# Kernel tuning notes

Measured on AMD Instinct MI355X. Metric: run time of the kernel, lower is better.

The kernel has to match this reference:

```python
import jax, jax.numpy as jnp
import numpy as np

WIN = 5            # attn.window_size
K = 2 * WIN + 1    # max local window width
NEG = -10000.0


def gru_cell(x, h, w_ih, w_hh, b_ih, b_hh):
    # torch GRU cell: r,z,n gate order
    gi = x @ w_ih.T + b_ih
    gh = h @ w_hh.T + b_hh
    ir, iz, inn = jnp.split(gi, 3, axis=-1)
    hr, hz, hn = jnp.split(gh, 3, axis=-1)
    r = jax.nn.sigmoid(ir + hr)
    z = jax.nn.sigmoid(iz + hz)
    n = jnp.tanh(inn + r * hn)
    return (1.0 - z) * n + z * h


def setup_inputs() -> dict:
    key = jax.random.key(0)
    ks = jax.random.split(key, 26)
    B, S, V, E, H, Hd = 64, 1024, 50257, 300, 1000, 500
    sc = 0.05
    dec_in = jax.random.randint(ks[0], (B, 1), 0, V)
    lengths = jax.random.randint(ks[1], (B,), 64, S + 1)
    mask0 = jnp.arange(S)[None, :] < lengths[:, None]          # [B,S] bool pad mask
    enc_out = jax.random.normal(ks[2], (B, S, H), jnp.float32)
    attn_hidden = jax.random.normal(ks[3], (B, 1, H), jnp.float32) * sc
    h0 = jax.random.normal(ks[4], (4, B, Hd), jnp.float32) * sc  # [layers*dirs,B,Hd]
    embed = jax.random.normal(ks[5], (V, E), jnp.float32) * sc
    embed = embed.at[0].set(0.0)  # padding_idx=0
    # GRU layer0 (input = E+H due to input feeding), layer1 (input = H)
    w_ih0 = jax.random.normal(ks[6], (2, 3 * Hd, E + H), jnp.float32) * sc
    w_hh0 = jax.random.normal(ks[7], (2, 3 * Hd, Hd), jnp.float32) * sc
    b_ih0 = jax.random.normal(ks[8], (2, 3 * Hd), jnp.float32) * sc
    b_hh0 = jax.random.normal(ks[9], (2, 3 * Hd), jnp.float32) * sc
    w_ih1 = jax.random.normal(ks[10], (2, 3 * Hd, H), jnp.float32) * sc
    w_hh1 = jax.random.normal(ks[11], (2, 3 * Hd, Hd), jnp.float32) * sc
    b_ih1 = jax.random.normal(ks[12], (2, 3 * Hd), jnp.float32) * sc
    b_hh1 = jax.random.normal(ks[13], (2, 3 * Hd), jnp.float32) * sc
    Wp_w = jax.random.normal(ks[14], (H, H), jnp.float32) * sc
    Wp_b = jax.random.normal(ks[15], (H,), jnp.float32) * sc
    Vp_w = jax.random.normal(ks[16], (H, 1), jnp.float32) * sc
    Vp_b = jax.random.normal(ks[17], (1,), jnp.float32) * sc
    Wc_w = jax.random.normal(ks[18], (2 * H, H), jnp.float32) * sc
    Wc_b = jax.random.normal(ks[19], (H,), jnp.float32) * sc
    out_w = jax.random.normal(ks[20], (H, V), jnp.float32) * sc
    out_b = jax.random.normal(ks[21], (V,), jnp.float32) * sc
    return {
        'dec_in': dec_in, 'attn_hidden': attn_hidden, 'enc_out': enc_out,
        'mask0': mask0, 'lengths': lengths, 'h0': h0, 'embed': embed,
        'w_ih0': w_ih0, 'w_hh0': w_hh0, 'b_ih0': b_ih0, 'b_hh0': b_hh0,
        'w_ih1': w_ih1, 'w_hh1': w_hh1, 'b_ih1': b_ih1, 'b_hh1': b_hh1,
        'Wp_w': Wp_w, 'Wp_b': Wp_b, 'Vp_w': Vp_w, 'Vp_b': Vp_b,
        'Wc_w': Wc_w, 'Wc_b': Wc_b, 'out_w': out_w, 'out_b': out_b, 't': 0,
    }


def reference(dec_in, attn_hidden, enc_out, mask0, lengths, h0, embed,
              w_ih0, w_hh0, b_ih0, b_hh0, w_ih1, w_hh1, b_ih1, b_hh1,
              Wp_w, Wp_b, Vp_w, Vp_b, Wc_w, Wc_b, out_w, out_b, t):
    Smax = enc_out.shape[1]
    # embed + input feeding (seq len of the decoder step is 1)
    x = jnp.concatenate([embed[dec_in[:, 0]], attn_hidden[:, 0]], axis=-1)  # [B,E+H]
    # 2-layer bidirectional GRU over a length-1 sequence (eval: no dropout)
    hf = gru_cell(x, h0[0], w_ih0[0], w_hh0[0], b_ih0[0], b_hh0[0])
    hb = gru_cell(x, h0[1], w_ih0[1], w_hh0[1], b_ih0[1], b_hh0[1])
    x1 = jnp.concatenate([hf, hb], axis=-1)                                  # [B,H]
    hf2 = gru_cell(x1, h0[2], w_ih1[0], w_hh1[0], b_ih1[0], b_hh1[0])
    hb2 = gru_cell(x1, h0[3], w_ih1[1], w_hh1[1], b_ih1[1], b_hh1[1])
    ht = jnp.concatenate([hf2, hb2], axis=-1)[:, None, :]                    # [B,1,H]
    # local-p predictive window: pt = int(S * sigmoid(Vp(tanh(Wp(ht)))))
    Sf = lengths.astype(ht.dtype)
    pt = (Sf * jax.nn.sigmoid(jnp.tanh(ht @ Wp_w + Wp_b) @ Vp_w + Vp_b).reshape(-1)).astype(jnp.int32)
    p0 = jnp.minimum(lengths - WIN, jnp.maximum(0, pt - WIN))                # [B]
    p1 = jnp.minimum(lengths, pt + 1 + WIN)
    idx = p0[:, None] + jnp.arange(K)                                        # [B,K]
    valid = idx < p1[:, None]
    idxc = jnp.clip(idx, 0, Smax - 1)
    hs_w = jnp.take_along_axis(enc_out, idxc[:, :, None], axis=1)            # [B,K,H] batched gather
    m_w = jnp.take_along_axis(mask0, idxc, axis=1) & valid                   # [B,K]
    # dot alignment + mask + softmax
    a = jnp.einsum('bod,bkd->bok', ht, hs_w)                                 # [B,1,K]
    a = jax.nn.softmax(jnp.where(m_w[:, None, :], a, NEG), axis=-1)
    c = jnp.einsum('bok,bkd->bod', a, hs_w)                                  # [B,1,H]
    h_attn = jnp.tanh(jnp.concatenate([c, ht], axis=-1) @ Wc_w + Wc_b)       # [B,1,H]
    y = (h_attn @ out_w + out_b)[:, 0]                                       # [B,V]
    return jax.nn.log_softmax(y, axis=-1)
```

## Files before the change

### kernel.cpp

```cpp
#include <hip/hip_runtime.h>
#include <hip/hip_bf16.h>
#include <math.h>

typedef __attribute__((ext_vector_type(8))) short bf16x8;
typedef __attribute__((ext_vector_type(4))) float f32x4;

__device__ __forceinline__ float sigmoidf_(float x){ return 1.f/(1.f + expf(-x)); }
__device__ __forceinline__ short f2bf(float x){
    union { __hip_bfloat16 h; short s; } u; u.h = __float2bfloat16(x); return u.s;
}
__device__ __forceinline__ float bf2f(short s){
    union { unsigned u; float f; } v; v.u = ((unsigned)(unsigned short)s) << 16; return v.f;
}

template<int TRANS, int BIAS>
__device__ __forceinline__ void mm_core(
    const short* __restrict__ Abf, const float* __restrict__ W,
    const float* __restrict__ bias, float* __restrict__ outP,
    int K, int Kp, int N, int ks0, int ks1, int nblk)
{
    const int lane = threadIdx.x & 63;
    const int wave = threadIdx.x >> 6;
    const int l16  = lane & 15;
    const int lg   = lane >> 4;
    const int n    = nblk*64 + wave*16 + l16;
    const int nc   = min(n, N-1);

    f32x4 acc[4];
#pragma unroll
    for (int mt = 0; mt < 4; mt++) acc[mt] = f32x4{0.f,0.f,0.f,0.f};

    for (int ks = ks0; ks < ks1; ks++) {
        const int kl = ks*32 + lg*8;
        const short* ap = Abf + (long)l16*Kp + kl;
        bf16x8 a0 = *(const bf16x8*)(ap);
        bf16x8 a1 = *(const bf16x8*)(ap + (long)16*Kp);
        bf16x8 a2 = *(const bf16x8*)(ap + (long)32*Kp);
        bf16x8 a3 = *(const bf16x8*)(ap + (long)48*Kp);
        float wv[8];
        if (TRANS) {
            const float* wr = W + (long)nc*K;
            if (kl + 8 <= K) {
                float4 f0 = *(const float4*)(wr + kl);
                float4 f1 = *(const float4*)(wr + kl + 4);
                wv[0]=f0.x; wv[1]=f0.y; wv[2]=f0.z; wv[3]=f0.w;
                wv[4]=f1.x; wv[5]=f1.y; wv[6]=f1.z; wv[7]=f1.w;
            } else {
#pragma unroll
                for (int j=0;j<8;j++) wv[j] = wr[min(kl+j, K-1)];
            }
        } else {
            const float* wk = W + (long)kl*(long)N + nc;
            if (kl + 8 <= K) {
#pragma unroll
                for (int j=0;j<8;j++) wv[j] = wk[(long)j*N];
            } else {
#pragma unroll
                for (int j=0;j<8;j++) wv[j] = (kl+j < K) ? wk[(long)j*N] : 0.f;
            }
        }
        bf16x8 b;
#pragma unroll
        for (int j=0;j<8;j++) b[j] = f2bf(wv[j]);

        acc[0] = __builtin_amdgcn_mfma_f32_16x16x32_bf16(a0, b, acc[0], 0, 0, 0);
        acc[1] = __builtin_amdgcn_mfma_f32_16x16x32_bf16(a1, b, acc[1], 0, 0, 0);
        acc[2] = __builtin_amdgcn_mfma_f32_16x16x32_bf16(a2, b, acc[2], 0, 0, 0);
        acc[3] = __builtin_amdgcn_mfma_f32_16x16x32_bf16(a3, b, acc[3], 0, 0, 0);
    }

    if (n < N) {
        const float bv = BIAS ? bias[n] : 0.f;
#pragma unroll
        for (int mt = 0; mt < 4; mt++) {
#pragma unroll
            for (int q = 0; q < 4; q++) {
                int row = mt*16 + lg*4 + q;
                outP[(long)row*N + n] = acc[mt][q] + bv;
            }
        }
    }
}

template<int TRANS>
__device__ __forceinline__ void mm_core4(
    const short* __restrict__ Ahi, const short* __restrict__ Alo,
    const float* __restrict__ W, float* __restrict__ outP,
    int K, int Kp, int N, int ks0, int ks1, int nblk)
{
    const int lane = threadIdx.x & 63;
    const int wave = threadIdx.x >> 6;
    const int l16  = lane & 15;
    const int lg   = lane >> 4;
    const int n    = nblk*64 + wave*16 + l16;
    const int nc   = min(n, N-1);

    f32x4 acc[4];
#pragma unroll
    for (int mt = 0; mt < 4; mt++) acc[mt] = f32x4{0.f,0.f,0.f,0.f};

    for (int ks = ks0; ks < ks1; ks++) {
        const int kl = ks*32 + lg*8;
        const long o0 = (long)l16*Kp + kl;
        bf16x8 ah0 = *(const bf16x8*)(Ahi + o0);
        bf16x8 ah1 = *(const bf16x8*)(Ahi + o0 + (long)16*Kp);
        bf16x8 ah2 = *(const bf16x8*)(Ahi + o0 + (long)32*Kp);
        bf16x8 ah3 = *(const bf16x8*)(Ahi + o0 + (long)48*Kp);
        bf16x8 al0 = *(const bf16x8*)(Alo + o0);
        bf16x8 al1 = *(const bf16x8*)(Alo + o0 + (long)16*Kp);
        bf16x8 al2 = *(const bf16x8*)(Alo + o0 + (long)32*Kp);
        bf16x8 al3 = *(const bf16x8*)(Alo + o0 + (long)48*Kp);
        float wv[8];
        if (TRANS) {
            const float* wr = W + (long)nc*K;
            if (kl + 8 <= K) {
                float4 f0 = *(const float4*)(wr + kl);
                float4 f1 = *(const float4*)(wr + kl + 4);
                wv[0]=f0.x; wv[1]=f0.y; wv[2]=f0.z; wv[3]=f0.w;
                wv[4]=f1.x; wv[5]=f1.y; wv[6]=f1.z; wv[7]=f1.w;
            } else {
#pragma unroll
                for (int j=0;j<8;j++) wv[j] = wr[min(kl+j, K-1)];
            }
        } else {
            const float* wk = W + (long)kl*(long)N + nc;
            if (kl + 8 <= K) {
#pragma unroll
                for (int j=0;j<8;j++) wv[j] = wk[(long)j*N];
            } else {
#pragma unroll
                for (int j=0;j<8;j++) wv[j] = (kl+j < K) ? wk[(long)j*N] : 0.f;
            }
        }
        bf16x8 bh, bl;
#pragma unroll
        for (int j=0;j<8;j++) {
            short h = f2bf(wv[j]);
            bh[j] = h;
            bl[j] = f2bf(wv[j] - bf2f(h));
        }
        acc[0] = __builtin_amdgcn_mfma_f32_16x16x32_bf16(ah0, bh, acc[0], 0, 0, 0);
        acc[1] = __builtin_amdgcn_mfma_f32_16x16x32_bf16(ah1, bh, acc[1], 0, 0, 0);
        acc[2] = __builtin_amdgcn_mfma_f32_16x16x32_bf16(ah2, bh, acc[2], 0, 0, 0);
        acc[3] = __builtin_amdgcn_mfma_f32_16x16x32_bf16(ah3, bh, acc[3], 0, 0, 0);
        acc[0] = __builtin_amdgcn_mfma_f32_16x16x32_bf16(ah0, bl, acc[0], 0, 0, 0);
        acc[1] = __builtin_amdgcn_mfma_f32_16x16x32_bf16(ah1, bl, acc[1], 0, 0, 0);
        acc[2] = __builtin_amdgcn_mfma_f32_16x16x32_bf16(ah2, bl, acc[2], 0, 0, 0);
        acc[3] = __builtin_amdgcn_mfma_f32_16x16x32_bf16(ah3, bl, acc[3], 0, 0, 0);
        acc[0] = __builtin_amdgcn_mfma_f32_16x16x32_bf16(al0, bh, acc[0], 0, 0, 0);
        acc[1] = __builtin_amdgcn_mfma_f32_16x16x32_bf16(al1, bh, acc[1], 0, 0, 0);
        acc[2] = __builtin_amdgcn_mfma_f32_16x16x32_bf16(al2, bh, acc[2], 0, 0, 0);
        acc[3] = __builtin_amdgcn_mfma_f32_16x16x32_bf16(al3, bh, acc[3], 0, 0, 0);
        acc[0] = __builtin_amdgcn_mfma_f32_16x16x32_bf16(al0, bl, acc[0], 0, 0, 0);
        acc[1] = __builtin_amdgcn_mfma_f32_16x16x32_bf16(al1, bl, acc[1], 0, 0, 0);
        acc[2] = __builtin_amdgcn_mfma_f32_16x16x32_bf16(al2, bl, acc[2], 0, 0, 0);
        acc[3] = __builtin_amdgcn_mfma_f32_16x16x32_bf16(al3, bl, acc[3], 0, 0, 0);
    }

    if (n < N) {
#pragma unroll
        for (int mt = 0; mt < 4; mt++) {
#pragma unroll
            for (int q = 0; q < 4; q++) {
                int row = mt*16 + lg*4 + q;
                outP[(long)row*N + n] = acc[mt][q];
            }
        }
    }
}

__global__ void k_prep(const int* __restrict__ dec_in, const float* __restrict__ attn_h,
                       const float* __restrict__ embed, const float* __restrict__ h0,
                       short* __restrict__ xhi, short* __restrict__ xlo,
                       short* __restrict__ h0hi, short* __restrict__ h0lo,
                       short* __restrict__ x1hi, short* __restrict__ x1lo,
                       short* __restrict__ hthi, short* __restrict__ htlo,
                       short* __restrict__ habf, short* __restrict__ catbf)
{
    int i = blockIdx.x*256 + threadIdx.x;
    if (i < 64*1312) {
        int b = i / 1312, k = i % 1312;
        float v = 0.f;
        if (k < 300)       v = embed[(long)dec_in[b]*300 + k];
        else if (k < 1300) v = attn_h[b*1000 + (k-300)];
        short h = f2bf(v);
        xhi[i] = h; xlo[i] = f2bf(v - bf2f(h));
        return;
    }
    i -= 64*1312;
    if (i < 4*64*512) {
        int d = i >> 15, r = i & 32767, b = r >> 9, k = r & 511;
        float v = (k < 500) ? h0[((long)d*64 + b)*500 + k] : 0.f;
        short h = f2bf(v);
        h0hi[i] = h; h0lo[i] = f2bf(v - bf2f(h));
        return;
    }
    i -= 4*64*512;
    if (i < 1536) {
        int b = i/24; long o = (long)b*1024 + 1000 + i%24;
        x1hi[o]=0; x1lo[o]=0; hthi[o]=0; htlo[o]=0; return;
    }
    i -= 1536;
    if (i < 1536) { int b = i/24; habf[(long)b*1024 + 1000 + i%24] = 0; return; }
    i -= 1536;
    if (i < 3072) { int b = i/48; catbf[(long)b*2048 + 2000 + i%48] = 0; return; }
}

template<int LAYER>
__global__ __launch_bounds__(256) void k_gru_mm(
    const short* __restrict__ Aih_hi, const short* __restrict__ Aih_lo,
    const short* __restrict__ h0hi,   const short* __restrict__ h0lo,
    const float* __restrict__ w_ih, const float* __restrict__ w_hh,
    float* __restrict__ Pgi, float* __restrict__ Pgh,
    int Kih, int Kpih, int Sih, int stepsih, int Shh, int stepshh)
{
    int z = blockIdx.z, s = blockIdx.y, nblk = blockIdx.x;
    if (z < 2) {
        if (s >= Sih) return;
        int nsteps = Kpih >> 5;
        int ks0 = s*stepsih, ks1 = min(nsteps, ks0 + stepsih);
        if (ks0 >= ks1) return;
        const float* W = w_ih + (long)z*1500*Kih;
        float* outP = Pgi + (long)(z*Sih + s)*96000;
        mm_core4<1>(Aih_hi, Aih_lo, W, outP, Kih, Kpih, 1500, ks0, ks1, nblk);
    } else {
        int d = z - 2;
        if (s >= Shh) return;
        int ks0 = s*stepshh, ks1 = min(16, ks0 + stepshh);
        if (ks0 >= ks1) return;
        const float* W = w_hh + (long)d*1500*500;
        float* outP = Pgh + (long)(d*Shh + s)*96000;
        const long ao = (long)(LAYER*2 + d)*64*512;
        mm_core4<1>(h0hi + ao, h0lo + ao, W, outP, 500, 512, 1500, ks0, ks1, nblk);
    }
}

__global__ __launch_bounds__(256) void k_nn_split4(
    const short* __restrict__ Ahi, const short* __restrict__ Alo,
    const float* __restrict__ W,
    float* __restrict__ P, int K, int Kp, int N, int steps)
{
    int s = blockIdx.y;
    int ks0 = s*steps, ks1 = min(Kp >> 5, ks0 + steps);
    if (ks0 >= ks1) return;
    mm_core4<0>(Ahi, Alo, W, P + (long)s*64*N, K, Kp, N, ks0, ks1, blockIdx.x);
}

__global__ __launch_bounds__(256) void k_nn_split(
    const short* __restrict__ Abf, const float* __restrict__ W,
    float* __restrict__ P, int K, int Kp, int N, int steps)
{
    int s = blockIdx.y;
    int ks0 = s*steps, ks1 = min(Kp >> 5, ks0 + steps);
    if (ks0 >= ks1) return;
    mm_core<0,0>(Abf, W, nullptr, P + (long)s*64*N, K, Kp, N, ks0, ks1, blockIdx.x);
}

__global__ __launch_bounds__(256) void k_out_mm(
    const short* __restrict__ Abf, const float* __restrict__ W,
    const float* __restrict__ bias, float* __restrict__ y,
    float* __restrict__ partS)
{
    const int N = 50257, K = 1000, Kp = 1024;
    const int lane = threadIdx.x & 63;
    const int wave = threadIdx.x >> 6;
    const int l16  = lane & 15;
    const int lg   = lane >> 4;
    const int nblk = blockIdx.x;
    const int n    = nblk*64 + wave*16 + l16;
    const bool ok  = n < N;
    const int nc   = ok ? n : (N-1);

    f32x4 acc[4];
#pragma unroll
    for (int mt = 0; mt < 4; mt++) acc[mt] = f32x4{0.f,0.f,0.f,0.f};

    for (int ks = 0; ks < 32; ks++) {
        const int kl = ks*32 + lg*8;
        const short* ap = Abf + (long)l16*Kp + kl;
        bf16x8 a0 = *(const bf16x8*)(ap);
        bf16x8 a1 = *(const bf16x8*)(ap + (long)16*Kp);
        bf16x8 a2 = *(const bf16x8*)(ap + (long)32*Kp);
        bf16x8 a3 = *(const bf16x8*)(ap + (long)48*Kp);
        float wv[8];
        const float* wk = W + (long)kl*(long)N + nc;
        if (kl + 8 <= K) {
#pragma unroll
            for (int j=0;j<8;j++) wv[j] = wk[(long)j*N];
        } else {
#pragma unroll
            for (int j=0;j<8;j++) wv[j] = (kl+j < K) ? wk[(long)j*N] : 0.f;
        }
        bf16x8 b;
#pragma unroll
        for (int j=0;j<8;j++) b[j] = f2bf(wv[j]);
        acc[0] = __builtin_amdgcn_mfma_f32_16x16x32_bf16(a0, b, acc[0], 0, 0, 0);
        acc[1] = __builtin_amdgcn_mfma_f32_16x16x32_bf16(a1, b, acc[1], 0, 0, 0);
        acc[2] = __builtin_amdgcn_mfma_f32_16x16x32_bf16(a2, b, acc[2], 0, 0, 0);
        acc[3] = __builtin_amdgcn_mfma_f32_16x16x32_bf16(a3, b, acc[3], 0, 0, 0);
    }

    __shared__ float psum[4][64];
    const float bv = ok ? bias[n] : 0.f;
#pragma unroll
    for (int mt = 0; mt < 4; mt++) {
#pragma unroll
        for (int q = 0; q < 4; q++) {
            int row = mt*16 + lg*4 + q;
            float v = acc[mt][q] + bv;
            if (ok) y[(long)row*N + n] = v;
            float e = ok ? expf(v) : 0.f;
            e += __shfl_xor(e, 1);
            e += __shfl_xor(e, 2);
            e += __shfl_xor(e, 4);
            e += __shfl_xor(e, 8);
            if (l16 == 0) psum[wave][row] = e;
        }
    }
    __syncthreads();
    int t = threadIdx.x;
    if (t < 64) partS[(long)t*786 + nblk] = psum[0][t] + psum[1][t] + psum[2][t] + psum[3][t];
}

__global__ void k_merge(const float* __restrict__ partS, float* __restrict__ lse)
{
    int t = threadIdx.x;
    int row = t & 63, seg = t >> 6;
    float s = 0.f;
    for (int p = seg; p < 786; p += 4) s += partS[(long)row*786 + p];
    __shared__ float red[256];
    red[t] = s;
    __syncthreads();
    if (t < 64) lse[row] = logf(red[row] + red[row+64] + red[row+128] + red[row+192]);
}

template<int LAYER>
__global__ void k_gates(const float* __restrict__ Pgi, const float* __restrict__ Pgh,
                        const float* __restrict__ h0,
                        const float* __restrict__ b_ih, const float* __restrict__ b_hh,
                        short* __restrict__ outhi, short* __restrict__ outlo,
                        float* __restrict__ ht, int SI, int SH)
{
    const int d = blockIdx.y;
    int i = blockIdx.x*256 + threadIdx.x;
    if (i >= 32000) return;
    int b = i / 500, q = i % 500;
    long base = (long)b*1500 + q;
    float g0 = b_ih[d*1500 + q], g1 = b_ih[d*1500 + 500 + q], g2 = b_ih[d*1500 + 1000 + q];
    for (int s = 0; s < SI; s++) {
        const float* P = Pgi + (long)(d*SI + s)*96000 + base;
        g0 += P[0]; g1 += P[500]; g2 += P[1000];
    }
    float h0v = b_hh[d*1500 + q], h1v = b_hh[d*1500 + 500 + q], h2v = b_hh[d*1500 + 1000 + q];
    for (int s = 0; s < SH; s++) {
        const float* P = Pgh + (long)(d*SH + s)*96000 + base;
        h0v += P[0]; h1v += P[500]; h2v += P[1000];
    }
    float hp = h0[((long)(LAYER*2 + d)*64 + b)*500 + q];
    float r = sigmoidf_(g0 + h0v);
    float z = sigmoidf_(g1 + h1v);
    float nn = tanhf(g2 + r*h2v);
    float o = (1.f - z)*nn + z*hp;
    long oo = (long)b*1024 + d*500 + q;
    short h = f2bf(o);
    outhi[oo] = h; outlo[oo] = f2bf(o - bf2f(h));
    if (LAYER == 1) ht[(long)b*1000 + d*500 + q] = o;
}

__global__ void k_attn(const float* __restrict__ enc, const float* __restrict__ ht,
                       const float* __restrict__ Pwp, const float* __restrict__ Wp_b,
                       const float* __restrict__ Vp_w, const float* __restrict__ Vp_b,
                       const int* __restrict__ lengths, short* __restrict__ catbf)
{
    int b = blockIdx.x;
    __shared__ float hts[1000];
    __shared__ float hs[11][1000];
    __shared__ float aa[16];
    __shared__ float red[4];
    __shared__ int sp[2];
    int tid = threadIdx.x;
    int lane = tid & 63, wave = tid >> 6;

    float ps = 0.f;
    for (int j = tid; j < 1000; j += 256) {
        float v = Wp_b[j];
#pragma unroll
        for (int s = 0; s < 8; s++) v += Pwp[(long)s*64000 + (long)b*1000 + j];
        ps += tanhf(v) * Vp_w[j];
    }
    for (int off = 32; off; off >>= 1) ps += __shfl_down(ps, off);
    if (lane == 0) red[wave] = ps;
    for (int h = tid; h < 1000; h += 256) hts[h] = ht[b*1000 + h];
    __syncthreads();
    if (tid == 0) {
        float tot = red[0] + red[1] + red[2] + red[3];
        float s = 1.f/(1.f + expf(-(tot + Vp_b[0])));
        int len = lengths[b];
        int pt = (int)((float)len * s);
        sp[0] = min(len - 5, max(0, pt - 5));
        sp[1] = min(len, pt + 6);
    }
    __syncthreads();
    int p0 = sp[0], p1 = sp[1];

    for (int k = 0; k < 11; k++) {
        int row = min(p0 + k, 1023);
        const float* er = enc + ((long)b*1024 + row)*1000;
        for (int h = tid; h < 1000; h += 256) hs[k][h] = er[h];
    }
    __syncthreads();
    for (int k = wave; k < 11; k += 4) {
        float d = 0.f;
        for (int h = lane; h < 1000; h += 64) d += hts[h]*hs[k][h];
        for (int off = 32; off; off >>= 1) d += __shfl_down(d, off);
        if (lane == 0) aa[k] = d;
    }
    __syncthreads();
    if (tid == 0) {
        int nv = min(p1 - p0, 11);
        float m = -1e30f;
        for (int k = 0; k < nv; k++) m = fmaxf(m, aa[k]);
        float ssum = 0.f;
        for (int k = 0; k < 11; k++) { float e = (k < nv) ? expf(aa[k]-m) : 0.f; aa[k] = e; ssum += e; }
        float inv = 1.f/ssum;
        for (int k = 0; k < 11; k++) aa[k] *= inv;
    }
    __syncthreads();
    for (int h = tid; h < 1000; h += 256) {
        float c = 0.f;
#pragma unroll
        for (int k = 0; k < 11; k++) c += aa[k]*hs[k][h];
        catbf[(long)b*2048 + h]        = f2bf(c);
        catbf[(long)b*2048 + 1000 + h] = f2bf(hts[h]);
    }
}

__global__ void k_hattn(const float* __restrict__ Pwc, const float* __restrict__ Wc_b,
                        short* __restrict__ habf, int S)
{
    int i = blockIdx.x*256 + threadIdx.x;
    if (i >= 64000) return;
    int b = i / 1000, nn = i % 1000;
    float v = Wc_b[nn];
    for (int s = 0; s < S; s++) v += Pwc[(long)s*64000 + i];
    habf[(long)b*1024 + nn] = f2bf(tanhf(v));
}

__global__ void k_sub(float* __restrict__ y, const float* __restrict__ lse)
{
    const int V = 50257;
    int b = blockIdx.y;
    int j = blockIdx.x*256 + threadIdx.x;
    if (j < V) y[(long)b*V + j] -= lse[b];
}

extern "C" void kernel_launch(void* const* d_in, const int* in_sizes, int n_in,
                              void* d_out, int out_size, void* d_ws, size_t ws_size,
                              hipStream_t stream)
{
    const int*   dec_in  = (const int*)  d_in[0];
    const float* attn_h  = (const float*)d_in[1];
    const float* enc     = (const float*)d_in[2];
    const int*   lengths = (const int*)  d_in[4];
    const float* h0      = (const float*)d_in[5];
    const float* embed   = (const float*)d_in[6];
    const float* w_ih0   = (const float*)d_in[7];
    const float* w_hh0   = (const float*)d_in[8];
    const float* b_ih0   = (const float*)d_in[9];
    const float* b_hh0   = (const float*)d_in[10];
    const float* w_ih1   = (const float*)d_in[11];
    const float* w_hh1   = (const float*)d_in[12];
    const float* b_ih1   = (const float*)d_in[13];
    const float* b_hh1   = (const float*)d_in[14];
    const float* Wp_w    = (const float*)d_in[15];
    const float* Wp_b    = (const float*)d_in[16];
    const float* Vp_w    = (const float*)d_in[17];
    const float* Vp_b    = (const float*)d_in[18];
    const float* Wc_w    = (const float*)d_in[19];
    const float* Wc_b    = (const float*)d_in[20];
    const float* out_w   = (const float*)d_in[21];
    const float* out_b   = (const float*)d_in[22];
    float* y = (float*)d_out;

    float* ws = (float*)d_ws;
    short* xhi   = (short*)(ws + 0);
    short* xlo   = (short*)(ws + 42000);
    short* h0hi  = (short*)(ws + 84000);
    short* h0lo  = (short*)(ws + 149600);
    short* x1hi  = (short*)(ws + 215200);
    short* x1lo  = (short*)(ws + 248000);
    short* hthi  = (short*)(ws + 280800);
    short* htlo  = (short*)(ws + 313600);
    short* catbf = (short*)(ws + 346400);
    short* habf  = (short*)(ws + 412000);
    float* ht    = ws + 444800;
    float* Pgi   = ws + 508800;
    float* Pgh   = ws + 1468800;
    float* Pwp   = ws + 1852800;
    float* Pwc   = ws + 2364800;
    float* partS = ws + 2876800;
    float* lse   = ws + 2927200;

    dim3 B256(256);

    k_prep<<<dim3((64*1312 + 4*64*512 + 1536 + 1536 + 3072 + 255)/256), B256, 0, stream>>>(
        dec_in, attn_h, embed, h0, xhi, xlo, h0hi, h0lo, x1hi, x1lo, hthi, htlo, habf, catbf);

    k_gru_mm<0><<<dim3(24, 5, 4), B256, 0, stream>>>(
        xhi, xlo, h0hi, h0lo, w_ih0, w_hh0, Pgi, Pgh, 1300, 1312, 5, 9, 2, 8);
    k_gates<0><<<dim3(125, 2), B256, 0, stream>>>(Pgi, Pgh, h0, b_ih0, b_hh0, x1hi, x1lo, ht, 5, 2);

    k_gru_mm<1><<<dim3(24, 4, 4), B256, 0, stream>>>(
        x1hi, x1lo, h0hi, h0lo, w_ih1, w_hh1, Pgi, Pgh, 1000, 1024, 4, 8, 2, 8);
    k_gates<1><<<dim3(125, 2), B256, 0, stream>>>(Pgi, Pgh, h0, b_ih1, b_hh1, hthi, htlo, ht, 4, 2);

    k_nn_split4<<<dim3(16, 8), B256, 0, stream>>>(hthi, htlo, Wp_w, Pwp, 1000, 1024, 1000, 4);

    k_attn<<<dim3(64), B256, 0, stream>>>(enc, ht, Pwp, Wp_b, Vp_w, Vp_b, lengths, catbf);
    k_nn_split<<<dim3(16, 8), B256, 0, stream>>>(catbf, Wc_w, Pwc, 2000, 2048, 1000, 8);
    k_hattn<<<dim3(250), B256, 0, stream>>>(Pwc, Wc_b, habf, 8);

    k_out_mm<<<dim3(786), B256, 0, stream>>>(habf, out_w, out_b, y, partS);
    k_merge<<<dim3(1), B256, 0, stream>>>(partS, lse);
    k_sub<<<dim3(197, 64), B256, 0, stream>>>(y, lse);
}
```

Baseline: 267.6 us.

## Fuse all decoder stages into one persistent kernel with grid barriers

Replaces the chain of about a dozen separate launches (prep, GRU matmuls, gates, projections, attention, output matmul, log-softmax merge and subtract) with a single persistent kernel of 512 blocks. A hand-rolled atomic grid barrier separates the phases. The layer-1 hidden-to-hidden matmuls are also hoisted into the first matmul phase, since they depend only on h0, which removes one dependency step. This aims to remove launch gaps and tail idle time between small kernels. In exchange it adds barrier latency, a large static LDS footprint that caps occupancy, and an uneven split of the 786 output-matmul tiles over 512 blocks. It also relies on all 512 blocks being co-resident, otherwise the barrier can deadlock.

```diff
diff --git a/kernel.cpp b/kernel.cpp
--- a/kernel.cpp
+++ b/kernel.cpp
@@ -5,6 +5,9 @@
 typedef __attribute__((ext_vector_type(8))) short bf16x8;
 typedef __attribute__((ext_vector_type(4))) float f32x4;
 
+#define NB 512
+#define NGRP 8
+
 __device__ __forceinline__ float sigmoidf_(float x){ return 1.f/(1.f + expf(-x)); }
 __device__ __forceinline__ short f2bf(float x){
     union { __hip_bfloat16 h; short s; } u; u.h = __float2bfloat16(x); return u.s;
@@ -13,8 +16,30 @@
     union { unsigned u; float f; } v; v.u = ((unsigned)(unsigned short)s) << 16; return v.f;
 }
 
+__device__ __forceinline__ void gbar(int* bar)
+{
+    __syncthreads();
+    if (threadIdx.x == 0) {
+        int gen = __hip_atomic_load(&bar[0], __ATOMIC_RELAXED, __HIP_MEMORY_SCOPE_AGENT);
+        int g = blockIdx.x >> 6;
+        int a = __hip_atomic_fetch_add(&bar[2+g], 1, __ATOMIC_ACQ_REL, __HIP_MEMORY_SCOPE_AGENT);
+        if (a == 63) {
+            __hip_atomic_store(&bar[2+g], 0, __ATOMIC_RELAXED, __HIP_MEMORY_SCOPE_AGENT);
+            int r = __hip_atomic_fetch_add(&bar[1], 1, __ATOMIC_ACQ_REL, __HIP_MEMORY_SCOPE_AGENT);
+            if (r == NGRP-1) {
+                __hip_atomic_store(&bar[1], 0, __ATOMIC_RELAXED, __HIP_MEMORY_SCOPE_AGENT);
+                __hip_atomic_fetch_add(&bar[0], 1, __ATOMIC_RELEASE, __HIP_MEMORY_SCOPE_AGENT);
+            }
+        }
+        while (__hip_atomic_load(&bar[0], __ATOMIC_RELAXED, __HIP_MEMORY_SCOPE_AGENT) == gen)
+            __builtin_amdgcn_s_sleep(2);
+        (void)__hip_atomic_load(&bar[0], __ATOMIC_ACQUIRE, __HIP_MEMORY_SCOPE_AGENT);
+    }
+    __syncthreads();
+}
+
 template<int TRANS, int BIAS>
-__device__ __forceinline__ void mm_core(
+__device__ void mm_core(
     const short* __restrict__ Abf, const float* __restrict__ W,
     const float* __restrict__ bias, float* __restrict__ outP,
     int K, int Kp, int N, int ks0, int ks1, int nblk)
@@ -83,7 +108,7 @@
 }
 
 template<int TRANS>
-__device__ __forceinline__ void mm_core4(
+__device__ void mm_core4(
     const short* __restrict__ Ahi, const short* __restrict__ Alo,
     const float* __restrict__ W, float* __restrict__ outP,
     int K, int Kp, int N, int ks0, int ks1, int nblk)
@@ -169,289 +194,298 @@
     }
 }
 
-__global__ void k_prep(const int* __restrict__ dec_in, const float* __restrict__ attn_h,
-                       const float* __restrict__ embed, const float* __restrict__ h0,
-                       short* __restrict__ xhi, short* __restrict__ xlo,
-                       short* __restrict__ h0hi, short* __restrict__ h0lo,
-                       short* __restrict__ x1hi, short* __restrict__ x1lo,
-                       short* __restrict__ hthi, short* __restrict__ htlo,
-                       short* __restrict__ habf, short* __restrict__ catbf)
+__global__ __launch_bounds__(256, 2) void k_mega(
+    const int* __restrict__ dec_in, const float* __restrict__ attn_h,
+    const float* __restrict__ enc,  const int* __restrict__ lengths,
+    const float* __restrict__ h0,   const float* __restrict__ embed,
+    const float* __restrict__ w_ih0, const float* __restrict__ w_hh0,
+    const float* __restrict__ b_ih0, const float* __restrict__ b_hh0,
+    const float* __restrict__ w_ih1, const float* __restrict__ w_hh1,
+    const float* __restrict__ b_ih1, const float* __restrict__ b_hh1,
+    const float* __restrict__ Wp_w, const float* __restrict__ Wp_b,
+    const float* __restrict__ Vp_w, const float* __restrict__ Vp_b,
+    const float* __restrict__ Wc_w, const float* __restrict__ Wc_b,
+    const float* __restrict__ out_w, const float* __restrict__ out_b,
+    float* __restrict__ y,
+    short* xhi, short* xlo, short* h0hi, short* h0lo,
+    short* x1hi, short* x1lo, short* hthi, short* htlo,
+    short* catbf, short* habf, float* ht,
+    float* PgiL0, float* PghL0, float* PgiL1, float* PghL1,
+    float* Pwp, float* Pwc, float* partS, float* lse, int* bar)
 {
-    int i = blockIdx.x*256 + threadIdx.x;
-    if (i < 64*1312) {
-        int b = i / 1312, k = i % 1312;
-        float v = 0.f;
-        if (k < 300)       v = embed[(long)dec_in[b]*300 + k];
-        else if (k < 1300) v = attn_h[b*1000 + (k-300)];
-        short h = f2bf(v);
-        xhi[i] = h; xlo[i] = f2bf(v - bf2f(h));
-        return;
-    }
-    i -= 64*1312;
-    if (i < 4*64*512) {
-        int d = i >> 15, r = i & 32767, b = r >> 9, k = r & 511;
-        float v = (k < 500) ? h0[((long)d*64 + b)*500 + k] : 0.f;
-        short h = f2bf(v);
-        h0hi[i] = h; h0lo[i] = f2bf(v - bf2f(h));
-        return;
-    }
-    i -= 4*64*512;
-    if (i < 1536) {
-        int b = i/24; long o = (long)b*1024 + 1000 + i%24;
-        x1hi[o]=0; x1lo[o]=0; hthi[o]=0; htlo[o]=0; return;
-    }
-    i -= 1536;
-    if (i < 1536) { int b = i/24; habf[(long)b*1024 + 1000 + i%24] = 0; return; }
-    i -= 1536;
-    if (i < 3072) { int b = i/48; catbf[(long)b*2048 + 2000 + i%48] = 0; return; }
-}
-
-template<int LAYER>
-__global__ __launch_bounds__(256) void k_gru_mm(
-    const short* __restrict__ Aih_hi, const short* __restrict__ Aih_lo,
-    const short* __restrict__ h0hi,   const short* __restrict__ h0lo,
-    const float* __restrict__ w_ih, const float* __restrict__ w_hh,
-    float* __restrict__ Pgi, float* __restrict__ Pgh,
-    int Kih, int Kpih, int Sih, int stepsih, int Shh, int stepshh)
-{
-    int z = blockIdx.z, s = blockIdx.y, nblk = blockIdx.x;
-    if (z < 2) {
-        if (s >= Sih) return;
-        int nsteps = Kpih >> 5;
-        int ks0 = s*stepsih, ks1 = min(nsteps, ks0 + stepsih);
-        if (ks0 >= ks1) return;
-        const float* W = w_ih + (long)z*1500*Kih;
-        float* outP = Pgi + (long)(z*Sih + s)*96000;
-        mm_core4<1>(Aih_hi, Aih_lo, W, outP, Kih, Kpih, 1500, ks0, ks1, nblk);
-    } else {
-        int d = z - 2;
-        if (s >= Shh) return;
-        int ks0 = s*stepshh, ks1 = min(16, ks0 + stepshh);
-        if (ks0 >= ks1) return;
-        const float* W = w_hh + (long)d*1500*500;
-        float* outP = Pgh + (long)(d*Shh + s)*96000;
-        const long ao = (long)(LAYER*2 + d)*64*512;
-        mm_core4<1>(h0hi + ao, h0lo + ao, W, outP, 500, 512, 1500, ks0, ks1, nblk);
-    }
-}
-
-__global__ __launch_bounds__(256) void k_nn_split4(
-    const short* __restrict__ Ahi, const short* __restrict__ Alo,
-    const float* __restrict__ W,
-    float* __restrict__ P, int K, int Kp, int N, int steps)
-{
-    int s = blockIdx.y;
-    int ks0 = s*steps, ks1 = min(Kp >> 5, ks0 + steps);
-    if (ks0 >= ks1) return;
-    mm_core4<0>(Ahi, Alo, W, P + (long)s*64*N, K, Kp, N, ks0, ks1, blockIdx.x);
-}
-
-__global__ __launch_bounds__(256) void k_nn_split(
-    const short* __restrict__ Abf, const float* __restrict__ W,
-    float* __restrict__ P, int K, int Kp, int N, int steps)
-{
-    int s = blockIdx.y;
-    int ks0 = s*steps, ks1 = min(Kp >> 5, ks0 + steps);
-    if (ks0 >= ks1) return;
-    mm_core<0,0>(Abf, W, nullptr, P + (long)s*64*N, K, Kp, N, ks0, ks1, blockIdx.x);
-}
-
-__global__ __launch_bounds__(256) void k_out_mm(
-    const short* __restrict__ Abf, const float* __restrict__ W,
-    const float* __restrict__ bias, float* __restrict__ y,
-    float* __restrict__ partS)
-{
-    const int N = 50257, K = 1000, Kp = 1024;
-    const int lane = threadIdx.x & 63;
-    const int wave = threadIdx.x >> 6;
-    const int l16  = lane & 15;
-    const int lg   = lane >> 4;
-    const int nblk = blockIdx.x;
-    const int n    = nblk*64 + wave*16 + l16;
-    const bool ok  = n < N;
-    const int nc   = ok ? n : (N-1);
-
-    f32x4 acc[4];
-#pragma unroll
-    for (int mt = 0; mt < 4; mt++) acc[mt] = f32x4{0.f,0.f,0.f,0.f};
-
-    for (int ks = 0; ks < 32; ks++) {
-        const int kl = ks*32 + lg*8;
-        const short* ap = Abf + (long)l16*Kp + kl;
-        bf16x8 a0 = *(const bf16x8*)(ap);
-        bf16x8 a1 = *(const bf16x8*)(ap + (long)16*Kp);
-        bf16x8 a2 = *(const bf16x8*)(ap + (long)32*Kp);
-        bf16x8 a3 = *(const bf16x8*)(ap + (long)48*Kp);
-        float wv[8];
-        const float* wk = W + (long)kl*(long)N + nc;
-        if (kl + 8 <= K) {
-#pragma unroll
-            for (int j=0;j<8;j++) wv[j] = wk[(long)j*N];
+    __shared__ float sm_hts[1000];
+    __shared__ float sm_hs[11][1000];
+    __shared__ float sm_aa[16];
+    __shared__ float sm_red[4];
+    __shared__ int   sm_p[2];
+    __shared__ float sm_ps[256];
+
+    const int tid  = threadIdx.x;
+    const int gtid = blockIdx.x*256 + tid;
+    const int lane = tid & 63, wave = tid >> 6;
+
+    for (int i = gtid; i < 221184; i += NB*256) {
+        int r = i;
+        if (r < 64*1312) {
+            int b = r / 1312, k = r % 1312;
+            float v = 0.f;
+            if (k < 300)       v = embed[(long)dec_in[b]*300 + k];
+            else if (k < 1300) v = attn_h[b*1000 + (k-300)];
+            short h = f2bf(v);
+            xhi[r] = h; xlo[r] = f2bf(v - bf2f(h));
+            continue;
+        }
+        r -= 64*1312;
+        if (r < 4*64*512) {
+            int k = r & 511, b = (r >> 9) & 63, d = r >> 15;
+            float v = (k < 500) ? h0[((long)d*64 + b)*500 + k] : 0.f;
+            short h = f2bf(v);
+            h0hi[r] = h; h0lo[r] = f2bf(v - bf2f(h));
+            continue;
+        }
+        r -= 4*64*512;
+        if (r < 1536) {
+            int b = r/24; long o = (long)b*1024 + 1000 + r%24;
+            x1hi[o]=0; x1lo[o]=0; hthi[o]=0; htlo[o]=0; continue;
+        }
+        r -= 1536;
+        if (r < 1536) { int b = r/24; habf[(long)b*1024 + 1000 + r%24] = 0; continue; }
+        r -= 1536;
+        { int b = r/48; catbf[(long)b*2048 + 2000 + r%48] = 0; }
+    }
+    gbar(bar);
+
+    for (int it = blockIdx.x; it < 432; it += NB) {
+        if (it < 240) {
+            int z = it / 120, rem = it % 120, s = rem / 24, nblk = rem % 24;
+            mm_core4<1>(xhi, xlo, w_ih0 + (long)z*1500*1300,
+                        PgiL0 + (long)(z*5 + s)*96000, 1300, 1312, 1500,
+                        s*9, min(41, s*9+9), nblk);
+        } else if (it < 336) {
+            int t = it - 240, d = t / 48, rem = t % 48, s = rem / 24, nblk = rem % 24;
+            const long ao = (long)(0*2 + d)*64*512;
+            mm_core4<1>(h0hi + ao, h0lo + ao, w_hh0 + (long)d*1500*500,
+                        PghL0 + (long)(d*2 + s)*96000, 500, 512, 1500,
+                        s*8, min(16, s*8+8), nblk);
         } else {
-#pragma unroll
-            for (int j=0;j<8;j++) wv[j] = (kl+j < K) ? wk[(long)j*N] : 0.f;
-        }
-        bf16x8 b;
-#pragma unroll
-        for (int j=0;j<8;j++) b[j] = f2bf(wv[j]);
-        acc[0] = __builtin_amdgcn_mfma_f32_16x16x32_bf16(a0, b, acc[0], 0, 0, 0);
-        acc[1] = __builtin_amdgcn_mfma_f32_16x16x32_bf16(a1, b, acc[1], 0, 0, 0);
-        acc[2] = __builtin_amdgcn_mfma_f32_16x16x32_bf16(a2, b, acc[2], 0, 0, 0);
-        acc[3] = __builtin_amdgcn_mfma_f32_16x16x32_bf16(a3, b, acc[3], 0, 0, 0);
-    }
-
-    __shared__ float psum[4][64];
-    const float bv = ok ? bias[n] : 0.f;
-#pragma unroll
-    for (int mt = 0; mt < 4; mt++) {
-#pragma unroll
-        for (int q = 0; q < 4; q++) {
-            int row = mt*16 + lg*4 + q;
-            float v = acc[mt][q] + bv;
-            if (ok) y[(long)row*N + n] = v;
-            float e = ok ? expf(v) : 0.f;
-            e += __shfl_xor(e, 1);
-            e += __shfl_xor(e, 2);
-            e += __shfl_xor(e, 4);
-            e += __shfl_xor(e, 8);
-            if (l16 == 0) psum[wave][row] = e;
-        }
-    }
-    __syncthreads();
-    int t = threadIdx.x;
-    if (t < 64) partS[(long)t*786 + nblk] = psum[0][t] + psum[1][t] + psum[2][t] + psum[3][t];
-}
-
-__global__ void k_merge(const float* __restrict__ partS, float* __restrict__ lse)
-{
-    int t = threadIdx.x;
-    int row = t & 63, seg = t >> 6;
-    float s = 0.f;
-    for (int p = seg; p < 786; p += 4) s += partS[(long)row*786 + p];
-    __shared__ float red[256];
-    red[t] = s;
-    __syncthreads();
-    if (t < 64) lse[row] = logf(red[row] + red[row+64] + red[row+128] + red[row+192]);
-}
-
-template<int LAYER>
-__global__ void k_gates(const float* __restrict__ Pgi, const float* __restrict__ Pgh,
-                        const float* __restrict__ h0,
-                        const float* __restrict__ b_ih, const float* __restrict__ b_hh,
-                        short* __restrict__ outhi, short* __restrict__ outlo,
-                        float* __restrict__ ht, int SI, int SH)
-{
-    const int d = blockIdx.y;
-    int i = blockIdx.x*256 + threadIdx.x;
-    if (i >= 32000) return;
-    int b = i / 500, q = i % 500;
-    long base = (long)b*1500 + q;
-    float g0 = b_ih[d*1500 + q], g1 = b_ih[d*1500 + 500 + q], g2 = b_ih[d*1500 + 1000 + q];
-    for (int s = 0; s < SI; s++) {
-        const float* P = Pgi + (long)(d*SI + s)*96000 + base;
-        g0 += P[0]; g1 += P[500]; g2 += P[1000];
-    }
-    float h0v = b_hh[d*1500 + q], h1v = b_hh[d*1500 + 500 + q], h2v = b_hh[d*1500 + 1000 + q];
-    for (int s = 0; s < SH; s++) {
-        const float* P = Pgh + (long)(d*SH + s)*96000 + base;
-        h0v += P[0]; h1v += P[500]; h2v += P[1000];
-    }
-    float hp = h0[((long)(LAYER*2 + d)*64 + b)*500 + q];
-    float r = sigmoidf_(g0 + h0v);
-    float z = sigmoidf_(g1 + h1v);
-    float nn = tanhf(g2 + r*h2v);
-    float o = (1.f - z)*nn + z*hp;
-    long oo = (long)b*1024 + d*500 + q;
-    short h = f2bf(o);
-    outhi[oo] = h; outlo[oo] = f2bf(o - bf2f(h));
-    if (LAYER == 1) ht[(long)b*1000 + d*500 + q] = o;
-}
-
-__global__ void k_attn(const float* __restrict__ enc, const float* __restrict__ ht,
-                       const float* __restrict__ Pwp, const float* __restrict__ Wp_b,
-                       const float* __restrict__ Vp_w, const float* __restrict__ Vp_b,
-                       const int* __restrict__ lengths, short* __restrict__ catbf)
-{
-    int b = blockIdx.x;
-    __shared__ float hts[1000];
-    __shared__ float hs[11][1000];
-    __shared__ float aa[16];
-    __shared__ float red[4];
-    __shared__ int sp[2];
-    int tid = threadIdx.x;
-    int lane = tid & 63, wave = tid >> 6;
-
-    float ps = 0.f;
-    for (int j = tid; j < 1000; j += 256) {
-        float v = Wp_b[j];
-#pragma unroll
-        for (int s = 0; s < 8; s++) v += Pwp[(long)s*64000 + (long)b*1000 + j];
-        ps += tanhf(v) * Vp_w[j];
-    }
-    for (int off = 32; off; off >>= 1) ps += __shfl_down(ps, off);
-    if (lane == 0) red[wave] = ps;
-    for (int h = tid; h < 1000; h += 256) hts[h] = ht[b*1000 + h];
-    __syncthreads();
-    if (tid == 0) {
-        float tot = red[0] + red[1] + red[2] + red[3];
-        float s = 1.f/(1.f + expf(-(tot + Vp_b[0])));
-        int len = lengths[b];
-        int pt = (int)((float)len * s);
-        sp[0] = min(len - 5, max(0, pt - 5));
-        sp[1] = min(len, pt + 6);
-    }
-    __syncthreads();
-    int p0 = sp[0], p1 = sp[1];
-
-    for (int k = 0; k < 11; k++) {
-        int row = min(p0 + k, 1023);
-        const float* er = enc + ((long)b*1024 + row)*1000;
-        for (int h = tid; h < 1000; h += 256) hs[k][h] = er[h];
-    }
-    __syncthreads();
-    for (int k = wave; k < 11; k += 4) {
-        float d = 0.f;
-        for (int h = lane; h < 1000; h += 64) d += hts[h]*hs[k][h];
-        for (int off = 32; off; off >>= 1) d += __shfl_down(d, off);
-        if (lane == 0) aa[k] = d;
-    }
-    __syncthreads();
-    if (tid == 0) {
-        int nv = min(p1 - p0, 11);
-        float m = -1e30f;
-        for (int k = 0; k < nv; k++) m = fmaxf(m, aa[k]);
-        float ssum = 0.f;
-        for (int k = 0; k < 11; k++) { float e = (k < nv) ? expf(aa[k]-m) : 0.f; aa[k] = e; ssum += e; }
-        float inv = 1.f/ssum;
-        for (int k = 0; k < 11; k++) aa[k] *= inv;
-    }
-    __syncthreads();
-    for (int h = tid; h < 1000; h += 256) {
-        float c = 0.f;
-#pragma unroll
-        for (int k = 0; k < 11; k++) c += aa[k]*hs[k][h];
-        catbf[(long)b*2048 + h]        = f2bf(c);
-        catbf[(long)b*2048 + 1000 + h] = f2bf(hts[h]);
-    }
-}
-
-__global__ void k_hattn(const float* __restrict__ Pwc, const float* __restrict__ Wc_b,
-                        short* __restrict__ habf, int S)
-{
-    int i = blockIdx.x*256 + threadIdx.x;
-    if (i >= 64000) return;
-    int b = i / 1000, nn = i % 1000;
-    float v = Wc_b[nn];
-    for (int s = 0; s < S; s++) v += Pwc[(long)s*64000 + i];
-    habf[(long)b*1024 + nn] = f2bf(tanhf(v));
-}
-
-__global__ void k_sub(float* __restrict__ y, const float* __restrict__ lse)
-{
-    const int V = 50257;
-    int b = blockIdx.y;
-    int j = blockIdx.x*256 + threadIdx.x;
-    if (j < V) y[(long)b*V + j] -= lse[b];
+            int t = it - 336, d = t / 48, rem = t % 48, s = rem / 24, nblk = rem % 24;
+            const long ao = (long)(1*2 + d)*64*512;
+            mm_core4<1>(h0hi + ao, h0lo + ao, w_hh1 + (long)d*1500*500,
+                        PghL1 + (long)(d*2 + s)*96000, 500, 512, 1500,
+                        s*8, min(16, s*8+8), nblk);
+        }
+    }
+    gbar(bar);
+
+    for (int i = gtid; i < 64000; i += NB*256) {
+        int d = i / 32000, r = i % 32000, b = r / 500, q = r % 500;
+        long base = (long)b*1500 + q;
+        float g0 = b_ih0[d*1500 + q], g1 = b_ih0[d*1500 + 500 + q], g2 = b_ih0[d*1500 + 1000 + q];
+        for (int s = 0; s < 5; s++) {
+            const float* P = PgiL0 + (long)(d*5 + s)*96000 + base;
+            g0 += P[0]; g1 += P[500]; g2 += P[1000];
+        }
+        float h0v = b_hh0[d*1500 + q], h1v = b_hh0[d*1500 + 500 + q], h2v = b_hh0[d*1500 + 1000 + q];
+        for (int s = 0; s < 2; s++) {
+            const float* P = PghL0 + (long)(d*2 + s)*96000 + base;
+            h0v += P[0]; h1v += P[500]; h2v += P[1000];
+        }
+        float hp = h0[((long)d*64 + b)*500 + q];
+        float rr = sigmoidf_(g0 + h0v);
+        float zz = sigmoidf_(g1 + h1v);
+        float nn = tanhf(g2 + rr*h2v);
+        float o = (1.f - zz)*nn + zz*hp;
+        long oo = (long)b*1024 + d*500 + q;
+        short h = f2bf(o);
+        x1hi[oo] = h; x1lo[oo] = f2bf(o - bf2f(h));
+    }
+    gbar(bar);
+
+    for (int it = blockIdx.x; it < 192; it += NB) {
+        int z = it / 96, rem = it % 96, s = rem / 24, nblk = rem % 24;
+        mm_core4<1>(x1hi, x1lo, w_ih1 + (long)z*1500*1000,
+                    PgiL1 + (long)(z*4 + s)*96000, 1000, 1024, 1500,
+                    s*8, min(32, s*8+8), nblk);
+    }
+    gbar(bar);
+
+    for (int i = gtid; i < 64000; i += NB*256) {
+        int d = i / 32000, r = i % 32000, b = r / 500, q = r % 500;
+        long base = (long)b*1500 + q;
+        float g0 = b_ih1[d*1500 + q], g1 = b_ih1[d*1500 + 500 + q], g2 = b_ih1[d*1500 + 1000 + q];
+        for (int s = 0; s < 4; s++) {
+            const float* P = PgiL1 + (long)(d*4 + s)*96000 + base;
+            g0 += P[0]; g1 += P[500]; g2 += P[1000];
+        }
+        float h0v = b_hh1[d*1500 + q], h1v = b_hh1[d*1500 + 500 + q], h2v = b_hh1[d*1500 + 1000 + q];
+        for (int s = 0; s < 2; s++) {
+            const float* P = PghL1 + (long)(d*2 + s)*96000 + base;
+            h0v += P[0]; h1v += P[500]; h2v += P[1000];
+        }
+        float hp = h0[((long)(2 + d)*64 + b)*500 + q];
+        float rr = sigmoidf_(g0 + h0v);
+        float zz = sigmoidf_(g1 + h1v);
+        float nn = tanhf(g2 + rr*h2v);
+        float o = (1.f - zz)*nn + zz*hp;
+        long oo = (long)b*1024 + d*500 + q;
+        short h = f2bf(o);
+        hthi[oo] = h; htlo[oo] = f2bf(o - bf2f(h));
+        ht[(long)b*1000 + d*500 + q] = o;
+    }
+    gbar(bar);
+
+    for (int it = blockIdx.x; it < 128; it += NB) {
+        int s = it / 16, nblk = it % 16;
+        mm_core4<0>(hthi, htlo, Wp_w, Pwp + (long)s*64000, 1000, 1024, 1000,
+                    s*4, min(32, s*4+4), nblk);
+    }
+    gbar(bar);
+
+    for (int b = blockIdx.x; b < 64; b += NB) {
+        float ps = 0.f;
+        for (int j = tid; j < 1000; j += 256) {
+            float v = Wp_b[j];
+#pragma unroll
+            for (int s = 0; s < 8; s++) v += Pwp[(long)s*64000 + (long)b*1000 + j];
+            ps += tanhf(v) * Vp_w[j];
+        }
+        for (int off = 32; off; off >>= 1) ps += __shfl_down(ps, off);
+        if (lane == 0) sm_red[wave] = ps;
+        for (int h = tid; h < 1000; h += 256) sm_hts[h] = ht[b*1000 + h];
+        __syncthreads();
+        if (tid == 0) {
+            float tot = sm_red[0] + sm_red[1] + sm_red[2] + sm_red[3];
+            float s = 1.f/(1.f + expf(-(tot + Vp_b[0])));
+            int len = lengths[b];
+            int pt = (int)((float)len * s);
+            sm_p[0] = min(len - 5, max(0, pt - 5));
+            sm_p[1] = min(len, pt + 6);
+        }
+        __syncthreads();
+        int p0 = sm_p[0], p1 = sm_p[1];
+        for (int k = 0; k < 11; k++) {
+            int row = min(p0 + k, 1023);
+            const float* er = enc + ((long)b*1024 + row)*1000;
+            for (int h = tid; h < 1000; h += 256) sm_hs[k][h] = er[h];
+        }
+        __syncthreads();
+        for (int k = wave; k < 11; k += 4) {
+            float d = 0.f;
+            for (int h = lane; h < 1000; h += 64) d += sm_hts[h]*sm_hs[k][h];
+            for (int off = 32; off; off >>= 1) d += __shfl_down(d, off);
+            if (lane == 0) sm_aa[k] = d;
+        }
+        __syncthreads();
+        if (tid == 0) {
+            int nv = min(p1 - p0, 11);
+            float m = -1e30f;
+            for (int k = 0; k < nv; k++) m = fmaxf(m, sm_aa[k]);
+            float ssum = 0.f;
+            for (int k = 0; k < 11; k++) { float e = (k < nv) ? expf(sm_aa[k]-m) : 0.f; sm_aa[k] = e; ssum += e; }
+            float inv = 1.f/ssum;
+            for (int k = 0; k < 11; k++) sm_aa[k] *= inv;
+        }
+        __syncthreads();
+        for (int h = tid; h < 1000; h += 256) {
+            float c = 0.f;
+#pragma unroll
+            for (int k = 0; k < 11; k++) c += sm_aa[k]*sm_hs[k][h];
+            catbf[(long)b*2048 + h]        = f2bf(c);
+            catbf[(long)b*2048 + 1000 + h] = f2bf(sm_hts[h]);
+        }
+        __syncthreads();
+    }
+    gbar(bar);
+
+    for (int it = blockIdx.x; it < 128; it += NB) {
+        int s = it / 16, nblk = it % 16;
+        mm_core<0,0>(catbf, Wc_w, nullptr, Pwc + (long)s*64000, 2000, 2048, 1000,
+                     s*8, s*8+8, nblk);
+    }
+    gbar(bar);
+
+    for (int i = gtid; i < 64000; i += NB*256) {
+        int b = i / 1000, nn = i % 1000;
+        float v = Wc_b[nn];
+        for (int s = 0; s < 8; s++) v += Pwc[(long)s*64000 + i];
+        habf[(long)b*1024 + nn] = f2bf(tanhf(v));
+    }
+    gbar(bar);
+
+    for (int nblk = blockIdx.x; nblk < 786; nblk += NB) {
+        const int N = 50257, K = 1000, Kp = 1024;
+        const int l16 = lane & 15, lg = lane >> 4;
+        const int n   = nblk*64 + wave*16 + l16;
+        const bool ok = n < N;
+        const int nc  = ok ? n : (N-1);
+
+        f32x4 acc[4];
+#pragma unroll
+        for (int mt = 0; mt < 4; mt++) acc[mt] = f32x4{0.f,0.f,0.f,0.f};
+
+        for (int ks = 0; ks < 32; ks++) {
+            const int kl = ks*32 + lg*8;
+            const short* ap = habf + (long)l16*Kp + kl;
+            bf16x8 a0 = *(const bf16x8*)(ap);
+            bf16x8 a1 = *(const bf16x8*)(ap + (long)16*Kp);
+            bf16x8 a2 = *(const bf16x8*)(ap + (long)32*Kp);
+            bf16x8 a3 = *(const bf16x8*)(ap + (long)48*Kp);
+            float wv[8];
+            const float* wk = out_w + (long)kl*(long)N + nc;
+            if (kl + 8 <= K) {
+#pragma unroll
+                for (int j=0;j<8;j++) wv[j] = wk[(long)j*N];
+            } else {
+#pragma unroll
+                for (int j=0;j<8;j++) wv[j] = (kl+j < K) ? wk[(long)j*N] : 0.f;
+            }
+            bf16x8 b;
+#pragma unroll
+            for (int j=0;j<8;j++) b[j] = f2bf(wv[j]);
+            acc[0] = __builtin_amdgcn_mfma_f32_16x16x32_bf16(a0, b, acc[0], 0, 0, 0);
+            acc[1] = __builtin_amdgcn_mfma_f32_16x16x32_bf16(a1, b, acc[1], 0, 0, 0);
+            acc[2] = __builtin_amdgcn_mfma_f32_16x16x32_bf16(a2, b, acc[2], 0, 0, 0);
+            acc[3] = __builtin_amdgcn_mfma_f32_16x16x32_bf16(a3, b, acc[3], 0, 0, 0);
+        }
+
+        const float bv = ok ? out_b[n] : 0.f;
+#pragma unroll
+        for (int mt = 0; mt < 4; mt++) {
+#pragma unroll
+            for (int q = 0; q < 4; q++) {
+                int row = mt*16 + lg*4 + q;
+                float v = acc[mt][q] + bv;
+                if (ok) y[(long)row*N + n] = v;
+                float e = ok ? expf(v) : 0.f;
+                e += __shfl_xor(e, 1);
+                e += __shfl_xor(e, 2);
+                e += __shfl_xor(e, 4);
+                e += __shfl_xor(e, 8);
+                if (l16 == 0) sm_ps[wave*64 + row] = e;
+            }
+        }
+        __syncthreads();
+        if (tid < 64)
+            partS[(long)tid*786 + nblk] = sm_ps[tid] + sm_ps[64+tid] + sm_ps[128+tid] + sm_ps[192+tid];
+        __syncthreads();
+    }
+    gbar(bar);
+
+    for (int row = blockIdx.x; row < 64; row += NB) {
+        float s = 0.f;
+        for (int p = tid; p < 786; p += 256) s += partS[(long)row*786 + p];
+        for (int off = 32; off; off >>= 1) s += __shfl_down(s, off);
+        if (lane == 0) sm_red[wave] = s;
+        __syncthreads();
+        if (tid == 0) lse[row] = logf(sm_red[0] + sm_red[1] + sm_red[2] + sm_red[3]);
+        __syncthreads();
+    }
+    gbar(bar);
+
+    for (int i = gtid; i < 64*50257; i += NB*256) {
+        int b = i / 50257;
+        y[i] -= lse[b];
+    }
 }
 
 extern "C" void kernel_launch(void* const* d_in, const int* in_sizes, int n_in,
@@ -494,33 +528,23 @@
     short* catbf = (short*)(ws + 346400);
     short* habf  = (short*)(ws + 412000);
     float* ht    = ws + 444800;
-    float* Pgi   = ws + 508800;
-    float* Pgh   = ws + 1468800;
-    float* Pwp   = ws + 1852800;
-    float* Pwc   = ws + 2364800;
-    float* partS = ws + 2876800;
-    float* lse   = ws + 2927200;
-
-    dim3 B256(256);
-
-    k_prep<<<dim3((64*1312 + 4*64*512 + 1536 + 1536 + 3072 + 255)/256), B256, 0, stream>>>(
-        dec_in, attn_h, embed, h0, xhi, xlo, h0hi, h0lo, x1hi, x1lo, hthi, htlo, habf, catbf);
-
-    k_gru_mm<0><<<dim3(24, 5, 4), B256, 0, stream>>>(
-        xhi, xlo, h0hi, h0lo, w_ih0, w_hh0, Pgi, Pgh, 1300, 1312, 5, 9, 2, 8);
-    k_gates<0><<<dim3(125, 2), B256, 0, stream>>>(Pgi, Pgh, h0, b_ih0, b_hh0, x1hi, x1lo, ht, 5, 2);
-
-    k_gru_mm<1><<<dim3(24, 4, 4), B256, 0, stream>>>(
-        x1hi, x1lo, h0hi, h0lo, w_ih1, w_hh1, Pgi, Pgh, 1000, 1024, 4, 8, 2, 8);
-    k_gates<1><<<dim3(125, 2), B256, 0, stream>>>(Pgi, Pgh, h0, b_ih1, b_hh1, hthi, htlo, ht, 4, 2);
-
-    k_nn_split4<<<dim3(16, 8), B256, 0, stream>>>(hthi, htlo, Wp_w, Pwp, 1000, 1024, 1000, 4);
-
-    k_attn<<<dim3(64), B256, 0, stream>>>(enc, ht, Pwp, Wp_b, Vp_w, Vp_b, lengths, catbf);
-    k_nn_split<<<dim3(16, 8), B256, 0, stream>>>(catbf, Wc_w, Pwc, 2000, 2048, 1000, 8);
-    k_hattn<<<dim3(250), B256, 0, stream>>>(Pwc, Wc_b, habf, 8);
-
-    k_out_mm<<<dim3(786), B256, 0, stream>>>(habf, out_w, out_b, y, partS);
-    k_merge<<<dim3(1), B256, 0, stream>>>(partS, lse);
-    k_sub<<<dim3(197, 64), B256, 0, stream>>>(y, lse);
-}
+    float* PgiL0 = ws + 508800;
+    float* PghL0 = ws + 1468800;
+    float* PgiL1 = ws + 1852800;
+    float* PghL1 = ws + 2620800;
+    float* Pwp   = ws + 3004800;
+    float* Pwc   = ws + 3516800;
+    float* partS = ws + 4028800;
+    float* lse   = ws + 4079200;
+    int*   bar   = (int*)(ws + 4079264);
+
+    hipMemsetAsync(bar, 0, 16*sizeof(int), stream);
+
+    k_mega<<<dim3(NB), dim3(256), 0, stream>>>(
+        dec_in, attn_h, enc, lengths, h0, embed,
+        w_ih0, w_hh0, b_ih0, b_hh0, w_ih1, w_hh1, b_ih1, b_hh1,
+        Wp_w, Wp_b, Vp_w, Vp_b, Wc_w, Wc_b, out_w, out_b, y,
+        xhi, xlo, h0hi, h0lo, x1hi, x1lo, hthi, htlo,
+        catbf, habf, ht, PgiL0, PghL0, PgiL1, PghL1,
+        Pwp, Pwc, partS, lse, bar);
+}
```

Result: slower. 701.6 us (+162.2%).
